# Kernel tuning notes

Hardware: AMD Instinct MI355X
Metric: run time of the kernel (lower is better)

The kernel has to match this reference:

```python
import jax, jax.numpy as jnp
import numpy as np

H = 2048          # hidden_size
F = 1408          # moe_intermediate_size
E = 64            # n_routed_experts
TOP_K = 6         # num_experts_per_tok
CAP = 512         # per-expert capacity (mean load ~192; overflow prob ~0)
SCALE = 1.0       # routed_scaling_factor
F_SH = 2 * F      # shared-expert intermediate (n_shared_experts=2)
B, S = 1, 2048


def setup_inputs() -> dict:
    key = jax.random.key(0)
    ks = jax.random.split(key, 8)
    s = 0.02
    return {
        "hidden_states": jax.random.normal(ks[0], (B, S, H), jnp.float32),
        "gate_w":  jax.random.normal(ks[1], (E, H), jnp.float32) * s,
        "w_gate":  jax.random.normal(ks[2], (E, H, F), jnp.float32) * s,
        "w_up":    jax.random.normal(ks[3], (E, H, F), jnp.float32) * s,
        "w_down":  jax.random.normal(ks[4], (E, F, H), jnp.float32) * s,
        "sh_gate": jax.random.normal(ks[5], (F_SH, H), jnp.float32) * s,
        "sh_up":   jax.random.normal(ks[6], (F_SH, H), jnp.float32) * s,
        "sh_down": jax.random.normal(ks[7], (H, F_SH), jnp.float32) * s,
    }


def reference(hidden_states, gate_w, w_gate, w_up, w_down, sh_gate, sh_up, sh_down):
    b, s, _ = hidden_states.shape
    x = hidden_states.reshape(-1, H)                       # [T, H]
    T = x.shape[0]

    # ---- gate: fp32 logits -> softmax -> top-k, scaled ----
    logits = x.astype(jnp.float32) @ gate_w.astype(jnp.float32).T   # [T, E]
    scores = jax.nn.softmax(logits, axis=-1)
    topk_w, topk_idx = jax.lax.top_k(scores, TOP_K)        # [T, K] (order irrelevant: summed)
    topk_w = topk_w * SCALE

    # ---- dispatch: sort expanded tokens by expert, scatter into [E, CAP, H] ----
    eid = topk_idx.reshape(-1)                             # [T*K]
    x_exp = jnp.repeat(x, TOP_K, axis=0)                   # [T*K, H] (token t repeated K times)
    order = jnp.argsort(eid)                               # stable sort by expert id
    eid_s = eid[order]
    counts = jnp.bincount(eid, length=E)
    starts = jnp.cumsum(counts) - counts                   # exclusive prefix sums
    pos = jnp.arange(T * TOP_K) - starts[eid_s]            # slot within expert
    valid = pos < CAP
    pos_c = jnp.where(valid, pos, CAP)                     # overflow -> scratch slot CAP
    buf = jnp.zeros((E, CAP + 1, H), x.dtype).at[eid_s, pos_c].set(x_exp[order])

    # ---- grouped expert SwiGLU MLP (grouped GEMM as batched einsum) ----
    g = jax.nn.silu(jnp.einsum('ech,ehf->ecf', buf, w_gate))
    u = jnp.einsum('ech,ehf->ecf', buf, w_up)
    d = jnp.einsum('ecf,efh->ech', g * u, w_down)          # [E, CAP+1, H]

    # ---- combine: gather, unsort, weighted sum over top-k ----
    out_s = jnp.where(valid[:, None], d[eid_s, pos_c], 0.0)
    out_exp = jnp.zeros_like(out_s).at[order].set(out_s)   # reverse_shuffle
    y = jnp.einsum('tkh,tk->th', out_exp.reshape(T, TOP_K, H), topk_w)
    y = y.astype(x.dtype).reshape(b, s, H)

    # ---- shared experts residual (dense SwiGLU MLP on identity) ----
    gs = jax.nn.silu(hidden_states @ sh_gate.T)
    us = hidden_states @ sh_up.T
    y = y + (gs * us) @ sh_down.T
    return y
```

## Files before the change

kernel.cpp:

```cpp
#include <hip/hip_runtime.h>
#include <hip/hip_bf16.h>

#define H 2048
#define FDIM 1408
#define NE 64
#define CAP 512
#define NTOK 2048
#define FSH 2816

typedef float  f32x4  __attribute__((ext_vector_type(4)));
typedef float  f32x2  __attribute__((ext_vector_type(2)));
typedef short  s16x8  __attribute__((ext_vector_type(8)));
typedef unsigned short u16;
typedef u16    u16x4v __attribute__((ext_vector_type(4)));

__device__ __forceinline__ u16 f2bf(float f) {
    union { float f; unsigned u; } v; v.f = f;
    unsigned u = v.u;
    u += 0x7fffu + ((u >> 16) & 1u);
    return (u16)(u >> 16);
}
__device__ __forceinline__ float bf2f(u16 b) {
    union { unsigned u; float f; } v; v.u = ((unsigned)b) << 16;
    return v.f;
}
__device__ __forceinline__ void glds16(const u16* g, u16* l) {
    __builtin_amdgcn_global_load_lds(
        (const __attribute__((address_space(1))) unsigned int*)g,
        (__attribute__((address_space(3))) unsigned int*)l, 16, 0, 0);
}

#define BAR() do { asm volatile("s_waitcnt lgkmcnt(0)" ::: "memory"); \
                   __builtin_amdgcn_s_barrier(); } while (0)
#define WAIT_VM(N)  asm volatile("s_waitcnt vmcnt(" #N ")" ::: "memory")
#define SCHED_FENCE() __builtin_amdgcn_sched_barrier(0)

__global__ __launch_bounds__(256) void xcvt(const float* __restrict__ x, u16* __restrict__ xb) {
    int i = blockIdx.x * 256 + threadIdx.x;
    const float4 a = ((const float4*)x)[2 * i];
    const float4 b = ((const float4*)x)[2 * i + 1];
    u16 v[8] = { f2bf(a.x), f2bf(a.y), f2bf(a.z), f2bf(a.w),
                 f2bf(b.x), f2bf(b.y), f2bf(b.z), f2bf(b.w) };
    *(s16x8*)(xb + (size_t)i * 8) = *(s16x8*)v;
}

__global__ void init_cnt(int* __restrict__ c) { c[threadIdx.x] = 0; }

__global__ __launch_bounds__(64) void gate_topk(
    const float* __restrict__ xg, const float* __restrict__ gw,
    int* __restrict__ cnt, int* __restrict__ tok_of,
    int* __restrict__ slot_enc, float* __restrict__ tw)
{
    const int t = blockIdx.x;
    const int lane = threadIdx.x;
    __shared__ float4 xs[512];
    const float4* xr = (const float4*)(xg + (size_t)t * H);
    #pragma unroll
    for (int i = 0; i < 8; ++i) xs[i * 64 + lane] = xr[i * 64 + lane];
    __syncthreads();

    const float4* gr = (const float4*)(gw + (size_t)lane * H);
    float acc = 0.f;
    #pragma unroll 4
    for (int i = 0; i < 512; ++i) {
        float4 a = xs[i], b = gr[i];
        acc += a.x * b.x + a.y * b.y + a.z * b.z + a.w * b.w;
    }
    float m = acc;
    #pragma unroll
    for (int off = 32; off; off >>= 1) m = fmaxf(m, __shfl_xor(m, off));
    float p = __expf(acc - m);
    float s = p;
    #pragma unroll
    for (int off = 32; off; off >>= 1) s += __shfl_xor(s, off);
    p = p / s;

    float myw = 0.f; int mye = 0;
    float v = p;
    for (int k = 0; k < 6; ++k) {
        float bv = v; int bi = lane;
        #pragma unroll
        for (int off = 32; off; off >>= 1) {
            float ov = __shfl_xor(bv, off);
            int   oi = __shfl_xor(bi, off);
            if (ov > bv || (ov == bv && oi < bi)) { bv = ov; bi = oi; }
        }
        if (lane == k)  { myw = bv; mye = bi; }
        if (lane == bi) v = -1.f;
    }
    if (lane < 6) {
        int slot = atomicAdd(&cnt[mye], 1);
        int enc = -1;
        if (slot < CAP) { tok_of[mye * CAP + slot] = t; enc = mye * CAP + slot; }
        slot_enc[t * 6 + lane] = enc;
        tw[t * 6 + lane] = myw;
    }
}

template<bool ROUTED>
__global__ __launch_bounds__(256, 3) void dual_gemm(
    const u16* __restrict__ xbf, const int* __restrict__ tok_of,
    const int* __restrict__ cnt_arr, const float* __restrict__ wg,
    const float* __restrict__ wu, u16* __restrict__ act, int Fd)
{
    __shared__ u16 As[2][256 * 32];
    __shared__ u16 Bgs[4 * 32 * 8];
    __shared__ u16 Bus[4 * 32 * 8];

    int e = 0, cnt, m0, f0;
    if constexpr (ROUTED) {
        e = blockIdx.z;
        cnt = cnt_arr[e]; cnt = cnt < CAP ? cnt : CAP;
        f0 = blockIdx.x * 32; m0 = blockIdx.y * 256;
        if (m0 >= cnt) return;
    } else {
        cnt = NTOK;
        m0 = blockIdx.x * 256; f0 = blockIdx.y * 32;
    }

    const float* wg_e = wg;
    const float* wu_e = wu;
    u16* act_e = act;
    if constexpr (ROUTED) {
        wg_e += (size_t)e * H * Fd;
        wu_e += (size_t)e * H * Fd;
        act_e += (size_t)e * CAP * Fd;
    }

    const int tid = threadIdx.x;
    const int lane = tid & 63;
    const int wv = tid >> 6;
    const int NT = H / 32;

    const int gA = ((lane & 3) ^ ((lane >> 3) & 3)) * 8;
    const u16* agp[4];
    #pragma unroll
    for (int q = 0; q < 4; ++q) {
        int rloc = (q * 4 + wv) * 16 + (lane >> 2);
        int srow = m0 + rloc;
        const u16* base;
        if constexpr (ROUTED) {
            const int* tok = tok_of + e * CAP;
            base = xbf + (size_t)tok[srow < cnt ? srow : 0] * H;
        } else {
            base = xbf + (size_t)srow * H;
        }
        agp[q] = base + gA;
    }
    const int mat = tid >> 7;
    const int bb = tid & 127;
    const float* bsrc;
    int n2 = 0, kq = 0, dr = 0, dcq = 0;
    if constexpr (ROUTED) {
        n2 = bb & 15; kq = bb >> 4;
        bsrc = (mat ? wu_e : wg_e) + (size_t)(kq * 4) * Fd + f0 + n2 * 2;
    } else {
        dr = bb >> 2; dcq = bb & 3;
        bsrc = (mat ? wu_e : wg_e) + (size_t)(f0 + dr) * H + dcq * 8;
    }

    f32x4 accg[4][2], accu[4][2];
    const f32x4 zero4 = {0.f, 0.f, 0.f, 0.f};
    #pragma unroll
    for (int i = 0; i < 4; ++i)
        #pragma unroll
        for (int j = 0; j < 2; ++j) { accg[i][j] = zero4; accu[i][j] = zero4; }

    f32x2 bR2[4];
    f32x4 bR4[2];

    auto GLDS_A = [&](int kt, int b) {
        #pragma unroll
        for (int q = 0; q < 4; ++q)
            glds16(agp[q] + kt * 32, &As[b][(q * 4 + wv) * 512]);
    };
    auto LOADB = [&](int kt) {
        if constexpr (ROUTED) {
            #pragma unroll
            for (int j = 0; j < 4; ++j)
                bR2[j] = *(const f32x2*)(bsrc + ((size_t)kt * 32 + j) * Fd);
        } else {
            bR4[0] = *(const f32x4*)(bsrc + kt * 32);
            bR4[1] = *(const f32x4*)(bsrc + kt * 32 + 4);
        }
    };
    auto STOREB = [&]() {
        u16* Bdst = mat ? Bus : Bgs;
        if constexpr (ROUTED) {
            #pragma unroll
            for (int c = 0; c < 2; ++c) {
                u16x4v v; v[0] = f2bf(bR2[0][c]); v[1] = f2bf(bR2[1][c]);
                          v[2] = f2bf(bR2[2][c]); v[3] = f2bf(bR2[3][c]);
                *(u16x4v*)&Bdst[(kq >> 1) * 256 + (n2 * 2 + c) * 8 + (kq & 1) * 4] = v;
            }
        } else {
            u16 v[8];
            v[0]=f2bf(bR4[0][0]); v[1]=f2bf(bR4[0][1]); v[2]=f2bf(bR4[0][2]); v[3]=f2bf(bR4[0][3]);
            v[4]=f2bf(bR4[1][0]); v[5]=f2bf(bR4[1][1]); v[6]=f2bf(bR4[1][2]); v[7]=f2bf(bR4[1][3]);
            *(s16x8*)&Bdst[dcq * 256 + dr * 8] = *(s16x8*)v;
        }
    };
    auto COMPUTE = [&](int b) {
        __builtin_amdgcn_s_setprio(1);
        const int j8 = lane >> 4;
        const int p8 = (j8 ^ ((lane >> 1) & 3)) * 8;
        s16x8 a[4], bg[2], bu[2];
        #pragma unroll
        for (int mi = 0; mi < 4; ++mi) {
            int r = wv * 64 + mi * 16 + (lane & 15);
            a[mi] = *(const s16x8*)&As[b][r * 32 + p8];
        }
        #pragma unroll
        for (int ni = 0; ni < 2; ++ni) {
            int c = ni * 16 + (lane & 15);
            bg[ni] = *(const s16x8*)&Bgs[j8 * 256 + c * 8];
            bu[ni] = *(const s16x8*)&Bus[j8 * 256 + c * 8];
        }
        #pragma unroll
        for (int mi = 0; mi < 4; ++mi)
            #pragma unroll
            for (int ni = 0; ni < 2; ++ni) {
                accg[mi][ni] = __builtin_amdgcn_mfma_f32_16x16x32_bf16(a[mi], bg[ni], accg[mi][ni], 0, 0, 0);
                accu[mi][ni] = __builtin_amdgcn_mfma_f32_16x16x32_bf16(a[mi], bu[ni], accu[mi][ni], 0, 0, 0);
            }
        __builtin_amdgcn_s_setprio(0);
    };

    GLDS_A(0, 0); SCHED_FENCE();
    LOADB(0);     SCHED_FENCE();
    STOREB();
    LOADB(1);     SCHED_FENCE();
    BAR(); SCHED_FENCE();

    for (int kt = 0; kt < NT; ++kt) {
        const int b = kt & 1;
        if (kt + 1 < NT) GLDS_A(kt + 1, b ^ 1);
        SCHED_FENCE();
        COMPUTE(b);
        BAR();
        if (kt + 1 < NT) {
            STOREB();
            if (kt + 2 < NT) LOADB(kt + 2);
        }
        SCHED_FENCE();
        if (kt + 1 < NT) {
            if (kt + 2 < NT) {
                if constexpr (ROUTED) { WAIT_VM(4); } else { WAIT_VM(2); }
            } else { WAIT_VM(0); }
        }
        BAR(); SCHED_FENCE();
    }

    #pragma unroll
    for (int mi = 0; mi < 4; ++mi)
        #pragma unroll
        for (int ni = 0; ni < 2; ++ni)
            #pragma unroll
            for (int r = 0; r < 4; ++r) {
                int srow = m0 + wv * 64 + mi * 16 + (lane >> 4) * 4 + r;
                if (srow < cnt) {
                    int fc = f0 + ni * 16 + (lane & 15);
                    float g = accg[mi][ni][r], u = accu[mi][ni][r];
                    float aa = (g / (1.f + __expf(-g))) * u;
                    act_e[(size_t)srow * Fd + fc] = f2bf(aa);
                }
            }
}

template<bool ROUTED>
__global__ __launch_bounds__(256, 3) void down_gemm(
    const u16* __restrict__ actA, const float* __restrict__ wdn,
    void* __restrict__ outp, const int* __restrict__ cnt_arr, int Kd)
{
    __shared__ u16 As[2][256 * 32];
    __shared__ u16 Bs[4 * 64 * 8];

    int e = 0, cnt, m0, n0;
    if constexpr (ROUTED) {
        e = blockIdx.z;
        cnt = cnt_arr[e]; cnt = cnt < CAP ? cnt : CAP;
        n0 = blockIdx.x * 64; m0 = blockIdx.y * 256;
        if (m0 >= cnt) return;
    } else {
        cnt = NTOK;
        m0 = blockIdx.x * 256; n0 = blockIdx.y * 64;
    }

    const u16* A_e = actA;
    const float* B_e = wdn;
    if constexpr (ROUTED) {
        A_e += (size_t)e * CAP * Kd;
        B_e += (size_t)e * Kd * H;
    }
    const int NT = Kd / 32;
    const int tid = threadIdx.x, lane = tid & 63, wv = tid >> 6;

    const int gA = ((lane & 3) ^ ((lane >> 3) & 3)) * 8;
    const u16* agp[4];
    #pragma unroll
    for (int q = 0; q < 4; ++q) {
        int rloc = (q * 4 + wv) * 16 + (lane >> 2);
        agp[q] = A_e + (size_t)(m0 + rloc) * Kd + gA;
    }
    const float* bsrc;
    int n2 = 0, kq = 0, dr = 0, dcq = 0;
    if constexpr (ROUTED) {
        n2 = tid & 31; kq = tid >> 5;
        bsrc = B_e + (size_t)(kq * 4) * H + n0 + n2 * 2;
    } else {
        dr = tid >> 2; dcq = tid & 3;
        bsrc = B_e + (size_t)(n0 + dr) * FSH + dcq * 8;
    }

    f32x4 acc[4][4];
    const f32x4 zero4 = {0.f, 0.f, 0.f, 0.f};
    #pragma unroll
    for (int i = 0; i < 4; ++i)
        #pragma unroll
        for (int j = 0; j < 4; ++j) acc[i][j] = zero4;

    f32x2 bR2[4];
    f32x4 bR4[2];

    auto GLDS_A = [&](int kt, int b) {
        #pragma unroll
        for (int q = 0; q < 4; ++q)
            glds16(agp[q] + kt * 32, &As[b][(q * 4 + wv) * 512]);
    };
    auto LOADB = [&](int kt) {
        if constexpr (ROUTED) {
            #pragma unroll
            for (int j = 0; j < 4; ++j)
                bR2[j] = *(const f32x2*)(bsrc + ((size_t)kt * 32 + j) * H);
        } else {
            bR4[0] = *(const f32x4*)(bsrc + kt * 32);
            bR4[1] = *(const f32x4*)(bsrc + kt * 32 + 4);
        }
    };
    auto STOREB = [&]() {
        if constexpr (ROUTED) {
            #pragma unroll
            for (int c = 0; c < 2; ++c) {
                u16x4v v; v[0] = f2bf(bR2[0][c]); v[1] = f2bf(bR2[1][c]);
                          v[2] = f2bf(bR2[2][c]); v[3] = f2bf(bR2[3][c]);
                *(u16x4v*)&Bs[(kq >> 1) * 512 + (n2 * 2 + c) * 8 + (kq & 1) * 4] = v;
            }
        } else {
            u16 v[8];
            v[0]=f2bf(bR4[0][0]); v[1]=f2bf(bR4[0][1]); v[2]=f2bf(bR4[0][2]); v[3]=f2bf(bR4[0][3]);
            v[4]=f2bf(bR4[1][0]); v[5]=f2bf(bR4[1][1]); v[6]=f2bf(bR4[1][2]); v[7]=f2bf(bR4[1][3]);
            *(s16x8*)&Bs[dcq * 512 + dr * 8] = *(s16x8*)v;
        }
    };
    auto COMPUTE = [&](int b) {
        __builtin_amdgcn_s_setprio(1);
        const int j8 = lane >> 4;
        const int p8 = (j8 ^ ((lane >> 1) & 3)) * 8;
        s16x8 a[4], bf[4];
        #pragma unroll
        for (int mi = 0; mi < 4; ++mi) {
            int r = wv * 64 + mi * 16 + (lane & 15);
            a[mi] = *(const s16x8*)&As[b][r * 32 + p8];
        }
        #pragma unroll
        for (int ni = 0; ni < 4; ++ni) {
            int c = ni * 16 + (lane & 15);
            bf[ni] = *(const s16x8*)&Bs[j8 * 512 + c * 8];
        }
        #pragma unroll
        for (int mi = 0; mi < 4; ++mi)
            #pragma unroll
            for (int ni = 0; ni < 4; ++ni)
                acc[mi][ni] = __builtin_amdgcn_mfma_f32_16x16x32_bf16(a[mi], bf[ni], acc[mi][ni], 0, 0, 0);
        __builtin_amdgcn_s_setprio(0);
    };

    GLDS_A(0, 0); SCHED_FENCE();
    LOADB(0);     SCHED_FENCE();
    STOREB();
    LOADB(1);     SCHED_FENCE();
    BAR(); SCHED_FENCE();

    for (int kt = 0; kt < NT; ++kt) {
        const int b = kt & 1;
        if (kt + 1 < NT) GLDS_A(kt + 1, b ^ 1);
        SCHED_FENCE();
        COMPUTE(b);
        BAR();
        if (kt + 1 < NT) {
            STOREB();
            if (kt + 2 < NT) LOADB(kt + 2);
        }
        SCHED_FENCE();
        if (kt + 1 < NT) {
            if (kt + 2 < NT) {
                if constexpr (ROUTED) { WAIT_VM(4); } else { WAIT_VM(2); }
            } else { WAIT_VM(0); }
        }
        BAR(); SCHED_FENCE();
    }

    #pragma unroll
    for (int mi = 0; mi < 4; ++mi)
        #pragma unroll
        for (int ni = 0; ni < 4; ++ni)
            #pragma unroll
            for (int r = 0; r < 4; ++r) {
                int srow = m0 + wv * 64 + mi * 16 + (lane >> 4) * 4 + r;
                if (srow < cnt) {
                    int col = n0 + ni * 16 + (lane & 15);
                    float vv = acc[mi][ni][r];
                    if constexpr (ROUTED)
                        ((u16*)outp)[(size_t)e * CAP * H + (size_t)srow * H + col] = f2bf(vv);
                    else
                        ((float*)outp)[(size_t)srow * H + col] = vv;
                }
            }
}

__global__ __launch_bounds__(256) void combine(
    float* __restrict__ y, const u16* __restrict__ d,
    const int* __restrict__ slot_enc, const float* __restrict__ tw)
{
    const int t = blockIdx.x, tid = threadIdx.x;
    int enc[6]; float w[6];
    #pragma unroll
    for (int k = 0; k < 6; ++k) {
        enc[k] = slot_enc[t * 6 + k];
        w[k] = tw[t * 6 + k];
    }
    float4* yrow = (float4*)(y + (size_t)t * H);
    #pragma unroll
    for (int it = 0; it < 2; ++it) {
        int h4 = it * 256 + tid;
        float4 acc = yrow[h4];
        #pragma unroll
        for (int k = 0; k < 6; ++k) {
            if (enc[k] >= 0) {
                ushort4 dv = ((const ushort4*)(d + (size_t)enc[k] * H))[h4];
                acc.x += w[k] * bf2f(dv.x);
                acc.y += w[k] * bf2f(dv.y);
                acc.z += w[k] * bf2f(dv.z);
                acc.w += w[k] * bf2f(dv.w);
            }
        }
        yrow[h4] = acc;
    }
}

extern "C" void kernel_launch(void* const* d_in, const int* in_sizes, int n_in,
                              void* d_out, int out_size, void* d_ws, size_t ws_size,
                              hipStream_t stream) {
    const float* x       = (const float*)d_in[0];
    const float* gw      = (const float*)d_in[1];
    const float* w_gate  = (const float*)d_in[2];
    const float* w_up    = (const float*)d_in[3];
    const float* w_down  = (const float*)d_in[4];
    const float* sh_gate = (const float*)d_in[5];
    const float* sh_up   = (const float*)d_in[6];
    const float* sh_down = (const float*)d_in[7];
    float* y = (float*)d_out;

    char* wsb = (char*)d_ws;
    int*   cnt      = (int*)(wsb + 0);
    int*   tok_of   = (int*)(wsb + 512);
    int*   slot_enc = (int*)(wsb + 512 + 131072);
    float* tw       = (float*)(wsb + 512 + 131072 + 49152);
    u16*   act      = (u16*)(wsb + 230144);
    u16*   actsh    = (u16*)(wsb + 230144 + 92274688);
    u16*   dbuf     = (u16*)(wsb + 230144 + 92274688 + 11534336);
    u16*   xbf      = dbuf;

    init_cnt<<<1, 64, 0, stream>>>(cnt);
    xcvt<<<NTOK * H / 8 / 256, 256, 0, stream>>>(x, xbf);
    gate_topk<<<NTOK, 64, 0, stream>>>(x, gw, cnt, tok_of, slot_enc, tw);
    dual_gemm<true><<<dim3(FDIM / 32, 2, NE), 256, 0, stream>>>(
        xbf, tok_of, cnt, w_gate, w_up, act, FDIM);
    dual_gemm<false><<<dim3(NTOK / 256, FSH / 32, 1), 256, 0, stream>>>(
        xbf, nullptr, nullptr, sh_gate, sh_up, actsh, FSH);
    down_gemm<true><<<dim3(H / 64, 2, NE), 256, 0, stream>>>(
        act, w_down, (void*)dbuf, cnt, FDIM);
    down_gemm<false><<<dim3(NTOK / 256, H / 64, 1), 256, 0, stream>>>(
        actsh, sh_down, (void*)y, nullptr, FSH);
    combine<<<NTOK, 256, 0, stream>>>(y, dbuf, slot_enc, tw);
}
```

Measured before the change: 1.110 ms.

## Load GEMM A operand directly into registers with double-buffered 64-wide K tiles

The routed and shared gate/up and down GEMMs no longer stage the bf16 activation operand in LDS through global_load_lds. Each wave instead loads its own A fragments from global memory straight into two alternating register buffers. The K tile grows from 32 to 64, so every LDS B tile holds twice as many k-groups and the main loop is unrolled by two. This removes the A LDS round trip and its explicit vmcnt waits, in exchange for much higher register pressure; down_gemm's occupancy hint drops from 3 to 2 blocks. Global latency hiding now depends on compiler-inserted waits.

```diff
diff --git a/kernel.cpp b/kernel.cpp
--- a/kernel.cpp
+++ b/kernel.cpp
@@ -24,15 +24,9 @@
     union { unsigned u; float f; } v; v.u = ((unsigned)b) << 16;
     return v.f;
 }
-__device__ __forceinline__ void glds16(const u16* g, u16* l) {
-    __builtin_amdgcn_global_load_lds(
-        (const __attribute__((address_space(1))) unsigned int*)g,
-        (__attribute__((address_space(3))) unsigned int*)l, 16, 0, 0);
-}
 
 #define BAR() do { asm volatile("s_waitcnt lgkmcnt(0)" ::: "memory"); \
                    __builtin_amdgcn_s_barrier(); } while (0)
-#define WAIT_VM(N)  asm volatile("s_waitcnt vmcnt(" #N ")" ::: "memory")
 #define SCHED_FENCE() __builtin_amdgcn_sched_barrier(0)
 
 __global__ __launch_bounds__(256) void xcvt(const float* __restrict__ x, u16* __restrict__ xb) {
@@ -103,9 +97,8 @@
     const int* __restrict__ cnt_arr, const float* __restrict__ wg,
     const float* __restrict__ wu, u16* __restrict__ act, int Fd)
 {
-    __shared__ u16 As[2][256 * 32];
-    __shared__ u16 Bgs[4 * 32 * 8];
-    __shared__ u16 Bus[4 * 32 * 8];
+    __shared__ u16 Bgs[8][32][8];
+    __shared__ u16 Bus[8][32][8];
 
     int e = 0, cnt, m0, f0;
     if constexpr (ROUTED) {
@@ -130,33 +123,30 @@
     const int tid = threadIdx.x;
     const int lane = tid & 63;
     const int wv = tid >> 6;
-    const int NT = H / 32;
-
-    const int gA = ((lane & 3) ^ ((lane >> 3) & 3)) * 8;
-    const u16* agp[4];
-    #pragma unroll
-    for (int q = 0; q < 4; ++q) {
-        int rloc = (q * 4 + wv) * 16 + (lane >> 2);
-        int srow = m0 + rloc;
-        const u16* base;
+    const int NT = H / 64;
+
+    const int kg = (lane >> 4) * 8;
+    const u16* ap[4];
+    #pragma unroll
+    for (int mi = 0; mi < 4; ++mi) {
+        int srow = m0 + wv * 64 + mi * 16 + (lane & 15);
         if constexpr (ROUTED) {
             const int* tok = tok_of + e * CAP;
-            base = xbf + (size_t)tok[srow < cnt ? srow : 0] * H;
+            ap[mi] = xbf + (size_t)tok[srow < cnt ? srow : 0] * H + kg;
         } else {
-            base = xbf + (size_t)srow * H;
-        }
-        agp[q] = base + gA;
+            ap[mi] = xbf + (size_t)srow * H + kg;
+        }
     }
     const int mat = tid >> 7;
     const int bb = tid & 127;
     const float* bsrc;
     int n2 = 0, kq = 0, dr = 0, dcq = 0;
     if constexpr (ROUTED) {
-        n2 = bb & 15; kq = bb >> 4;
+        n2 = bb & 15; kq = bb >> 3 & 0xF; kq = bb >> 4;
         bsrc = (mat ? wu_e : wg_e) + (size_t)(kq * 4) * Fd + f0 + n2 * 2;
     } else {
         dr = bb >> 2; dcq = bb & 3;
-        bsrc = (mat ? wu_e : wg_e) + (size_t)(f0 + dr) * H + dcq * 8;
+        bsrc = (mat ? wu_e : wg_e) + (size_t)(f0 + dr) * H + dcq * 16;
     }
 
     f32x4 accg[4][2], accu[4][2];
@@ -166,88 +156,101 @@
         #pragma unroll
         for (int j = 0; j < 2; ++j) { accg[i][j] = zero4; accu[i][j] = zero4; }
 
-    f32x2 bR2[4];
-    f32x4 bR4[2];
-
-    auto GLDS_A = [&](int kt, int b) {
-        #pragma unroll
-        for (int q = 0; q < 4; ++q)
-            glds16(agp[q] + kt * 32, &As[b][(q * 4 + wv) * 512]);
+    s16x8 aA0[8], aA1[8];
+    f32x2 bR2[8];
+    f32x4 bR4[4];
+
+    auto LOADA = [&](int kt, s16x8 (&a)[8]) {
+        #pragma unroll
+        for (int kk = 0; kk < 2; ++kk)
+            #pragma unroll
+            for (int mi = 0; mi < 4; ++mi)
+                a[kk * 4 + mi] = *(const s16x8*)(ap[mi] + kt * 64 + kk * 32);
     };
     auto LOADB = [&](int kt) {
         if constexpr (ROUTED) {
             #pragma unroll
-            for (int j = 0; j < 4; ++j)
-                bR2[j] = *(const f32x2*)(bsrc + ((size_t)kt * 32 + j) * Fd);
+            for (int j = 0; j < 4; ++j) {
+                bR2[j]     = *(const f32x2*)(bsrc + ((size_t)kt * 64 + j) * Fd);
+                bR2[4 + j] = *(const f32x2*)(bsrc + ((size_t)kt * 64 + 32 + j) * Fd);
+            }
         } else {
-            bR4[0] = *(const f32x4*)(bsrc + kt * 32);
-            bR4[1] = *(const f32x4*)(bsrc + kt * 32 + 4);
+            #pragma unroll
+            for (int q = 0; q < 4; ++q)
+                bR4[q] = *(const f32x4*)(bsrc + kt * 64 + q * 4);
         }
     };
     auto STOREB = [&]() {
-        u16* Bdst = mat ? Bus : Bgs;
+        u16* Bdst = mat ? &Bus[0][0][0] : &Bgs[0][0][0];
         if constexpr (ROUTED) {
             #pragma unroll
             for (int c = 0; c < 2; ++c) {
-                u16x4v v; v[0] = f2bf(bR2[0][c]); v[1] = f2bf(bR2[1][c]);
-                          v[2] = f2bf(bR2[2][c]); v[3] = f2bf(bR2[3][c]);
-                *(u16x4v*)&Bdst[(kq >> 1) * 256 + (n2 * 2 + c) * 8 + (kq & 1) * 4] = v;
+                u16x4v v0, v1;
+                #pragma unroll
+                for (int j = 0; j < 4; ++j) { v0[j] = f2bf(bR2[j][c]); v1[j] = f2bf(bR2[4 + j][c]); }
+                *(u16x4v*)&Bdst[((kq >> 1)) * 256 + (n2 * 2 + c) * 8 + (kq & 1) * 4] = v0;
+                *(u16x4v*)&Bdst[(4 + (kq >> 1)) * 256 + (n2 * 2 + c) * 8 + (kq & 1) * 4] = v1;
             }
         } else {
-            u16 v[8];
-            v[0]=f2bf(bR4[0][0]); v[1]=f2bf(bR4[0][1]); v[2]=f2bf(bR4[0][2]); v[3]=f2bf(bR4[0][3]);
-            v[4]=f2bf(bR4[1][0]); v[5]=f2bf(bR4[1][1]); v[6]=f2bf(bR4[1][2]); v[7]=f2bf(bR4[1][3]);
-            *(s16x8*)&Bdst[dcq * 256 + dr * 8] = *(s16x8*)v;
-        }
-    };
-    auto COMPUTE = [&](int b) {
+            #pragma unroll
+            for (int q = 0; q < 4; ++q) {
+                u16x4v v;
+                v[0] = f2bf(bR4[q][0]); v[1] = f2bf(bR4[q][1]);
+                v[2] = f2bf(bR4[q][2]); v[3] = f2bf(bR4[q][3]);
+                *(u16x4v*)&Bdst[(dcq * 2 + (q >> 1)) * 256 + dr * 8 + (q & 1) * 4] = v;
+            }
+        }
+    };
+    auto COMPUTE = [&](const s16x8 (&a)[8]) {
         __builtin_amdgcn_s_setprio(1);
         const int j8 = lane >> 4;
-        const int p8 = (j8 ^ ((lane >> 1) & 3)) * 8;
-        s16x8 a[4], bg[2], bu[2];
-        #pragma unroll
-        for (int mi = 0; mi < 4; ++mi) {
-            int r = wv * 64 + mi * 16 + (lane & 15);
-            a[mi] = *(const s16x8*)&As[b][r * 32 + p8];
-        }
-        #pragma unroll
-        for (int ni = 0; ni < 2; ++ni) {
-            int c = ni * 16 + (lane & 15);
-            bg[ni] = *(const s16x8*)&Bgs[j8 * 256 + c * 8];
-            bu[ni] = *(const s16x8*)&Bus[j8 * 256 + c * 8];
-        }
-        #pragma unroll
-        for (int mi = 0; mi < 4; ++mi)
+        #pragma unroll
+        for (int kk = 0; kk < 2; ++kk) {
+            const int g = kk * 4 + j8;
+            s16x8 bg[2], bu[2];
             #pragma unroll
             for (int ni = 0; ni < 2; ++ni) {
-                accg[mi][ni] = __builtin_amdgcn_mfma_f32_16x16x32_bf16(a[mi], bg[ni], accg[mi][ni], 0, 0, 0);
-                accu[mi][ni] = __builtin_amdgcn_mfma_f32_16x16x32_bf16(a[mi], bu[ni], accu[mi][ni], 0, 0, 0);
-            }
+                int c = ni * 16 + (lane & 15);
+                bg[ni] = *(const s16x8*)&Bgs[g][c][0];
+                bu[ni] = *(const s16x8*)&Bus[g][c][0];
+            }
+            #pragma unroll
+            for (int mi = 0; mi < 4; ++mi)
+                #pragma unroll
+                for (int ni = 0; ni < 2; ++ni) {
+                    accg[mi][ni] = __builtin_amdgcn_mfma_f32_16x16x32_bf16(a[kk * 4 + mi], bg[ni], accg[mi][ni], 0, 0, 0);
+                    accu[mi][ni] = __builtin_amdgcn_mfma_f32_16x16x32_bf16(a[kk * 4 + mi], bu[ni], accu[mi][ni], 0, 0, 0);
+                }
+        }
         __builtin_amdgcn_s_setprio(0);
     };
 
-    GLDS_A(0, 0); SCHED_FENCE();
-    LOADB(0);     SCHED_FENCE();
+    LOADA(0, aA0);
+    LOADB(0);
     STOREB();
-    LOADB(1);     SCHED_FENCE();
+    LOADB(1);
     BAR(); SCHED_FENCE();
 
-    for (int kt = 0; kt < NT; ++kt) {
-        const int b = kt & 1;
-        if (kt + 1 < NT) GLDS_A(kt + 1, b ^ 1);
-        SCHED_FENCE();
-        COMPUTE(b);
+    for (int kt = 0; kt < NT; kt += 2) {
+        if (kt + 1 < NT) LOADA(kt + 1, aA1);
+        SCHED_FENCE();
+        COMPUTE(aA0);
         BAR();
         if (kt + 1 < NT) {
             STOREB();
             if (kt + 2 < NT) LOADB(kt + 2);
         }
         SCHED_FENCE();
-        if (kt + 1 < NT) {
-            if (kt + 2 < NT) {
-                if constexpr (ROUTED) { WAIT_VM(4); } else { WAIT_VM(2); }
-            } else { WAIT_VM(0); }
-        }
+        BAR(); SCHED_FENCE();
+        if (kt + 2 < NT) LOADA(kt + 2, aA0);
+        SCHED_FENCE();
+        COMPUTE(aA1);
+        BAR();
+        if (kt + 2 < NT) {
+            STOREB();
+            if (kt + 3 < NT) LOADB(kt + 3);
+        }
+        SCHED_FENCE();
         BAR(); SCHED_FENCE();
     }
 
@@ -268,12 +271,11 @@
 }
 
 template<bool ROUTED>
-__global__ __launch_bounds__(256, 3) void down_gemm(
+__global__ __launch_bounds__(256, 2) void down_gemm(
     const u16* __restrict__ actA, const float* __restrict__ wdn,
     void* __restrict__ outp, const int* __restrict__ cnt_arr, int Kd)
 {
-    __shared__ u16 As[2][256 * 32];
-    __shared__ u16 Bs[4 * 64 * 8];
+    __shared__ u16 Bs[8][64][8];
 
     int e = 0, cnt, m0, n0;
     if constexpr (ROUTED) {
@@ -292,15 +294,15 @@
         A_e += (size_t)e * CAP * Kd;
         B_e += (size_t)e * Kd * H;
     }
-    const int NT = Kd / 32;
+    const int NT = Kd / 64;
     const int tid = threadIdx.x, lane = tid & 63, wv = tid >> 6;
 
-    const int gA = ((lane & 3) ^ ((lane >> 3) & 3)) * 8;
-    const u16* agp[4];
-    #pragma unroll
-    for (int q = 0; q < 4; ++q) {
-        int rloc = (q * 4 + wv) * 16 + (lane >> 2);
-        agp[q] = A_e + (size_t)(m0 + rloc) * Kd + gA;
+    const int kg = (lane >> 4) * 8;
+    const u16* ap[4];
+    #pragma unroll
+    for (int mi = 0; mi < 4; ++mi) {
+        int srow = m0 + wv * 64 + mi * 16 + (lane & 15);
+        ap[mi] = A_e + (size_t)srow * Kd + kg;
     }
     const float* bsrc;
     int n2 = 0, kq = 0, dr = 0, dcq = 0;
@@ -309,7 +311,7 @@
         bsrc = B_e + (size_t)(kq * 4) * H + n0 + n2 * 2;
     } else {
         dr = tid >> 2; dcq = tid & 3;
-        bsrc = B_e + (size_t)(n0 + dr) * FSH + dcq * 8;
+        bsrc = B_e + (size_t)(n0 + dr) * FSH + dcq * 16;
     }
 
     f32x4 acc[4][4];
@@ -319,84 +321,95 @@
         #pragma unroll
         for (int j = 0; j < 4; ++j) acc[i][j] = zero4;
 
-    f32x2 bR2[4];
-    f32x4 bR4[2];
-
-    auto GLDS_A = [&](int kt, int b) {
-        #pragma unroll
-        for (int q = 0; q < 4; ++q)
-            glds16(agp[q] + kt * 32, &As[b][(q * 4 + wv) * 512]);
+    s16x8 aA0[8], aA1[8];
+    f32x2 bR2[8];
+    f32x4 bR4[4];
+
+    auto LOADA = [&](int kt, s16x8 (&a)[8]) {
+        #pragma unroll
+        for (int kk = 0; kk < 2; ++kk)
+            #pragma unroll
+            for (int mi = 0; mi < 4; ++mi)
+                a[kk * 4 + mi] = *(const s16x8*)(ap[mi] + kt * 64 + kk * 32);
     };
     auto LOADB = [&](int kt) {
         if constexpr (ROUTED) {
             #pragma unroll
-            for (int j = 0; j < 4; ++j)
-                bR2[j] = *(const f32x2*)(bsrc + ((size_t)kt * 32 + j) * H);
+            for (int j = 0; j < 4; ++j) {
+                bR2[j]     = *(const f32x2*)(bsrc + ((size_t)kt * 64 + j) * H);
+                bR2[4 + j] = *(const f32x2*)(bsrc + ((size_t)kt * 64 + 32 + j) * H);
+            }
         } else {
-            bR4[0] = *(const f32x4*)(bsrc + kt * 32);
-            bR4[1] = *(const f32x4*)(bsrc + kt * 32 + 4);
+            #pragma unroll
+            for (int q = 0; q < 4; ++q)
+                bR4[q] = *(const f32x4*)(bsrc + kt * 64 + q * 4);
         }
     };
     auto STOREB = [&]() {
         if constexpr (ROUTED) {
             #pragma unroll
             for (int c = 0; c < 2; ++c) {
-                u16x4v v; v[0] = f2bf(bR2[0][c]); v[1] = f2bf(bR2[1][c]);
-                          v[2] = f2bf(bR2[2][c]); v[3] = f2bf(bR2[3][c]);
-                *(u16x4v*)&Bs[(kq >> 1) * 512 + (n2 * 2 + c) * 8 + (kq & 1) * 4] = v;
+                u16x4v v0, v1;
+                #pragma unroll
+                for (int j = 0; j < 4; ++j) { v0[j] = f2bf(bR2[j][c]); v1[j] = f2bf(bR2[4 + j][c]); }
+                *(u16x4v*)&Bs[(kq >> 1)][n2 * 2 + c][(kq & 1) * 4] = v0;
+                *(u16x4v*)&Bs[4 + (kq >> 1)][n2 * 2 + c][(kq & 1) * 4] = v1;
             }
         } else {
-            u16 v[8];
-            v[0]=f2bf(bR4[0][0]); v[1]=f2bf(bR4[0][1]); v[2]=f2bf(bR4[0][2]); v[3]=f2bf(bR4[0][3]);
-            v[4]=f2bf(bR4[1][0]); v[5]=f2bf(bR4[1][1]); v[6]=f2bf(bR4[1][2]); v[7]=f2bf(bR4[1][3]);
-            *(s16x8*)&Bs[dcq * 512 + dr * 8] = *(s16x8*)v;
-        }
-    };
-    auto COMPUTE = [&](int b) {
+            #pragma unroll
+            for (int q = 0; q < 4; ++q) {
+                u16x4v v;
+                v[0] = f2bf(bR4[q][0]); v[1] = f2bf(bR4[q][1]);
+                v[2] = f2bf(bR4[q][2]); v[3] = f2bf(bR4[q][3]);
+                *(u16x4v*)&Bs[dcq * 2 + (q >> 1)][dr][(q & 1) * 4] = v;
+            }
+        }
+    };
+    auto COMPUTE = [&](const s16x8 (&a)[8]) {
         __builtin_amdgcn_s_setprio(1);
         const int j8 = lane >> 4;
-        const int p8 = (j8 ^ ((lane >> 1) & 3)) * 8;
-        s16x8 a[4], bf[4];
-        #pragma unroll
-        for (int mi = 0; mi < 4; ++mi) {
-            int r = wv * 64 + mi * 16 + (lane & 15);
-            a[mi] = *(const s16x8*)&As[b][r * 32 + p8];
-        }
-        #pragma unroll
-        for (int ni = 0; ni < 4; ++ni) {
-            int c = ni * 16 + (lane & 15);
-            bf[ni] = *(const s16x8*)&Bs[j8 * 512 + c * 8];
-        }
-        #pragma unroll
-        for (int mi = 0; mi < 4; ++mi)
+        #pragma unroll
+        for (int kk = 0; kk < 2; ++kk) {
+            const int g = kk * 4 + j8;
+            s16x8 bf[4];
             #pragma unroll
             for (int ni = 0; ni < 4; ++ni)
-                acc[mi][ni] = __builtin_amdgcn_mfma_f32_16x16x32_bf16(a[mi], bf[ni], acc[mi][ni], 0, 0, 0);
+                bf[ni] = *(const s16x8*)&Bs[g][ni * 16 + (lane & 15)][0];
+            #pragma unroll
+            for (int mi = 0; mi < 4; ++mi)
+                #pragma unroll
+                for (int ni = 0; ni < 4; ++ni)
+                    acc[mi][ni] = __builtin_amdgcn_mfma_f32_16x16x32_bf16(a[kk * 4 + mi], bf[ni], acc[mi][ni], 0, 0, 0);
+        }
         __builtin_amdgcn_s_setprio(0);
     };
 
-    GLDS_A(0, 0); SCHED_FENCE();
-    LOADB(0);     SCHED_FENCE();
+    LOADA(0, aA0);
+    LOADB(0);
     STOREB();
-    LOADB(1);     SCHED_FENCE();
+    LOADB(1);
     BAR(); SCHED_FENCE();
 
-    for (int kt = 0; kt < NT; ++kt) {
-        const int b = kt & 1;
-        if (kt + 1 < NT) GLDS_A(kt + 1, b ^ 1);
-        SCHED_FENCE();
-        COMPUTE(b);
+    for (int kt = 0; kt < NT; kt += 2) {
+        if (kt + 1 < NT) LOADA(kt + 1, aA1);
+        SCHED_FENCE();
+        COMPUTE(aA0);
         BAR();
         if (kt + 1 < NT) {
             STOREB();
             if (kt + 2 < NT) LOADB(kt + 2);
         }
         SCHED_FENCE();
-        if (kt + 1 < NT) {
-            if (kt + 2 < NT) {
-                if constexpr (ROUTED) { WAIT_VM(4); } else { WAIT_VM(2); }
-            } else { WAIT_VM(0); }
-        }
+        BAR(); SCHED_FENCE();
+        if (kt + 2 < NT) LOADA(kt + 2, aA0);
+        SCHED_FENCE();
+        COMPUTE(aA1);
+        BAR();
+        if (kt + 2 < NT) {
+            STOREB();
+            if (kt + 3 < NT) LOADB(kt + 3);
+        }
+        SCHED_FENCE();
         BAR(); SCHED_FENCE();
     }
 
```

Measured after the change: 3.041 ms. 2.74x slower.
